# Kernel tuning notes

Hardware: AMD Instinct MI355X
Metric: run time of the kernel (lower is better)

The kernel has to match this reference:

```python
import jax, jax.numpy as jnp
import numpy as np

B, T, D = 2, 2048, 1024
K, F = 8, 4096
LAMBDA = 0.5


def setup_inputs() -> dict:
    key = jax.random.key(0)
    ks = jax.random.split(key, 8)
    s = 0.02
    return {
        "x": jax.random.normal(ks[0], (B, T, D), dtype=jnp.float32),
        "prev_logits": jax.random.normal(ks[1], (B, T, K), dtype=jnp.float32),
        "Wt": jax.random.normal(ks[2], (D, K), dtype=jnp.float32) * s,
        "Wgt": jax.random.normal(ks[3], (K, K), dtype=jnp.float32) * s,
        "We_logits": jnp.zeros((K,), dtype=jnp.float32),
        "W1": jax.random.normal(ks[4], (K, D, F), dtype=jnp.float32) * s,
        "b1": jnp.zeros((K, F), dtype=jnp.float32),
        "W2": jax.random.normal(ks[5], (K, F, D), dtype=jnp.float32) * s,
        "b2": jnp.zeros((K, D), dtype=jnp.float32),
    }


def reference(x, prev_logits, Wt, Wgt, We_logits, W1, b1, W2, b2):
    # gating: softmax over router logits, sigmoid-threshold multi-hot mask
    logits = jnp.einsum("btd,dk->btk", x, Wt) + jnp.einsum("btk,kj->btj", prev_logits, Wgt)
    st = jax.nn.softmax(logits, axis=-1)                       # (B,T,K)
    We = jax.nn.sigmoid(We_logits)                             # (K,)
    mask = (st > LAMBDA * We).astype(x.dtype)                  # (B,T,K)
    g = st * mask
    sel_counts = mask.sum(axis=(0, 1))                         # (K,)
    avg_density = mask.sum(axis=-1).mean()                     # scalar

    # dense multi-expert FFN: every expert on every token (dropout=0 / eval)
    h = jax.nn.gelu(jnp.einsum("btd,kdf->bktf", x, W1) + b1[:, None, :], approximate=False)
    outk = jnp.einsum("bktf,kfd->bktd", h, W2) + b2[:, None, :]  # (B,K,T,D)
    y = jnp.einsum("btk,bktd->btd", g, outk)
    y = y / (g.sum(axis=-1, keepdims=True) + 1e-6)
    return y, jax.lax.stop_gradient(logits), sel_counts, avg_density
```

## Files before the change

kernel.cpp:

```cpp
#include <hip/hip_runtime.h>
#include <cstdint>
#include <cstddef>

#define NB 2
#define NTT 2048
#define ND 1024
#define NK 8
#define NF 4096
#define NTOK (NB*NTT)
#define LAMBDA_C 0.5f

#define Y_SZ   (NTOK*ND)
#define LG_OFF Y_SZ
#define SC_OFF (LG_OFF + NTOK*NK)
#define AD_OFF (SC_OFF + NK)

#define WS_CNT    0
#define WS_SEG    8
#define WS_NTILES 17
#define WS_TILEK  32
#define WS_TILER  1056
#define WS_PTOK   4096
#define WS_PCOEF  36864
#define WS_COEF   69632
#define WS_X16    102400
#define WS_H      2199552

#define BM 128
#define BN 128
#define BK 64
#define SPLITK2 4

typedef float  f32x4 __attribute__((ext_vector_type(4)));
typedef _Float16 f16x8 __attribute__((ext_vector_type(8)));
typedef unsigned int u32x2 __attribute__((ext_vector_type(2)));
typedef unsigned int u32x4 __attribute__((ext_vector_type(4)));

__device__ __forceinline__ unsigned int pkrtz(float a, float b){
    auto h = __builtin_amdgcn_cvt_pkrtz(a, b);
    return __builtin_bit_cast(unsigned int, h);
}
__device__ __forceinline__ float gelu_exact(float v){
    return 0.5f * v * (1.0f + erff(v * 0.70710678118654752440f));
}

__global__ __launch_bounds__(256) void k_xcast(const float* __restrict__ x,
                                               unsigned short* __restrict__ x16)
{
    int i = (blockIdx.x*256 + threadIdx.x) * 16;
    const f32x4* src = (const f32x4*)(x + i);
    f32x4 v0 = src[0], v1 = src[1], v2 = src[2], v3 = src[3];
    u32x4 o0 = {pkrtz(v0[0],v0[1]), pkrtz(v0[2],v0[3]), pkrtz(v1[0],v1[1]), pkrtz(v1[2],v1[3])};
    u32x4 o1 = {pkrtz(v2[0],v2[1]), pkrtz(v2[2],v2[3]), pkrtz(v3[0],v3[1]), pkrtz(v3[2],v3[3])};
    *(u32x4*)(x16 + i)     = o0;
    *(u32x4*)(x16 + i + 8) = o1;
}

__global__ __launch_bounds__(256) void k_gating(
    const float* __restrict__ x, const float* __restrict__ pl,
    const float* __restrict__ Wt, const float* __restrict__ Wgt,
    const float* __restrict__ Wel, float* __restrict__ out,
    float* __restrict__ coef, int* __restrict__ cnt)
{
    int t = blockIdx.x;
    const float* xt = x + (size_t)t * ND;
    float acc[NK] = {0,0,0,0,0,0,0,0};
    for (int d = threadIdx.x; d < ND; d += 256){
        float xv = xt[d];
        const float4* w = (const float4*)(Wt + (size_t)d * NK);
        float4 w0 = w[0], w1 = w[1];
        acc[0] += xv*w0.x; acc[1] += xv*w0.y; acc[2] += xv*w0.z; acc[3] += xv*w0.w;
        acc[4] += xv*w1.x; acc[5] += xv*w1.y; acc[6] += xv*w1.z; acc[7] += xv*w1.w;
    }
    __shared__ float red[4][NK];
    #pragma unroll
    for (int k = 0; k < NK; k++){
        float v = acc[k];
        #pragma unroll
        for (int off = 32; off; off >>= 1) v += __shfl_down(v, off);
        if ((threadIdx.x & 63) == 0) red[threadIdx.x >> 6][k] = v;
    }
    __syncthreads();
    if (threadIdx.x == 0){
        const float* p = pl + (size_t)t * NK;
        float pv[NK];
        #pragma unroll
        for (int j = 0; j < NK; j++) pv[j] = p[j];
        float lg[NK]; float mx = -1e30f;
        #pragma unroll
        for (int k = 0; k < NK; k++){
            float v = red[0][k] + red[1][k] + red[2][k] + red[3][k];
            #pragma unroll
            for (int j = 0; j < NK; j++) v += pv[j] * Wgt[j*NK + k];
            lg[k] = v; mx = fmaxf(mx, v);
            out[LG_OFF + (size_t)t*NK + k] = v;
        }
        float e[NK]; float s = 0.f;
        #pragma unroll
        for (int k = 0; k < NK; k++){ e[k] = expf(lg[k] - mx); s += e[k]; }
        float g[NK]; float gsum = 0.f;
        #pragma unroll
        for (int k = 0; k < NK; k++){
            float st = e[k] / s;
            float we = 1.f / (1.f + expf(-Wel[k]));
            bool m = st > LAMBDA_C * we;
            g[k] = m ? st : 0.f;
            gsum += g[k];
        }
        float inv = 1.f / (gsum + 1e-6f);
        #pragma unroll
        for (int k = 0; k < NK; k++){
            coef[(size_t)t*NK + k] = g[k] * inv;
            if (g[k] > 0.f) atomicAdd(&cnt[k], 1);
        }
    }
}

__global__ __launch_bounds__(256) void k_scan(
    const float* __restrict__ coef, int* __restrict__ wsi,
    float* __restrict__ wsf, int pair_cap)
{
    int k = blockIdx.x;
    const int* cnt = wsi + WS_CNT;
    int base = 0;
    for (int j = 0; j < k; j++) base += cnt[j];
    int tid = threadIdx.x, lane = tid & 63, w = tid >> 6;
    __shared__ int wsum[4];
    __shared__ int sbase;
    if (tid == 0){
        sbase = base;
        wsi[WS_SEG + k] = base;
        if (k == NK-1) wsi[WS_SEG + NK] = base + cnt[k];
    }
    __syncthreads();
    int* ptok = wsi + WS_PTOK;
    float* pc = wsf + WS_PCOEF;
    for (int c0 = 0; c0 < NTOK; c0 += 256){
        int t = c0 + tid;
        float c = coef[(size_t)t*NK + k];
        bool m = c > 0.f;
        unsigned long long bal = __ballot(m);
        int pre = __popcll(bal & ((1ull << lane) - 1ull));
        if (lane == 0) wsum[w] = __popcll(bal);
        __syncthreads();
        int b = sbase;
        for (int j = 0; j < w; j++) b += wsum[j];
        if (m){
            int pos = b + pre;
            if (pos < pair_cap){ ptok[pos] = t; pc[pos] = c; }
        }
        __syncthreads();
        if (tid == 0) sbase += wsum[0] + wsum[1] + wsum[2] + wsum[3];
        __syncthreads();
    }
}

__global__ void k_tiles(int* __restrict__ wsi, float* __restrict__ out, int pair_cap)
{
    if (threadIdx.x == 0 && blockIdx.x == 0){
        const int* cnt = wsi + WS_CNT;
        const int* seg = wsi + WS_SEG;
        int total = 0;
        for (int k = 0; k < NK; k++){ total += cnt[k]; out[SC_OFF + k] = (float)cnt[k]; }
        out[AD_OFF] = (float)total / (float)NTOK;
        int nt = 0;
        for (int k = 0; k < NK; k++){
            int e = min(seg[k+1], pair_cap);
            for (int r = seg[k]; r < e; r += BM){
                wsi[WS_TILEK + nt] = k; wsi[WS_TILER + nt] = r; nt++;
            }
        }
        wsi[WS_NTILES] = nt;
    }
}

#define XCD_PART_LOOP(nwork)                                              \
    int q_ = (nwork) >> 3, rr_ = (nwork) & 7;                             \
    int xcd_ = blockIdx.x & 7;                                            \
    int slot_ = blockIdx.x >> 3;                                          \
    int nslot_ = gridDim.x >> 3;                                          \
    int cntw_ = q_ + (xcd_ < rr_ ? 1 : 0);                                \
    int start_ = xcd_ * q_ + (xcd_ < rr_ ? xcd_ : rr_);                   \
    for (int p_ = slot_; p_ < cntw_; p_ += nslot_)

#define LOAD_A16(ptr_)                                                    \
    { _Pragma("unroll")                                                   \
      for (int g_ = 0; g_ < 4; g_++) pa[g_] = *(const u32x4*)((ptr_) + g_*8); }

#define STAGE_A_F16()                                                     \
    { _Pragma("unroll")                                                   \
      for (int g_ = 0; g_ < 4; g_++){                                     \
          unsigned off_ = ((unsigned)((axkh*4 + g_)*16)) ^ aswz;          \
          *(u32x4*)(&lds[arowb + off_]) = pa[g_];                         \
      } }

#define STAGE_B_CVT(lb_)                                                  \
    {                                                                     \
        _Pragma("unroll")                                                 \
        for (int i_ = 0; i_ < 2; i_++){                                   \
            unsigned wA_[4], wB_[4];                                      \
            _Pragma("unroll")                                             \
            for (int r2_ = 0; r2_ < 4; r2_++){                            \
                wA_[r2_] = pkrtz(lb_[i_*4+r2_][0], lb_[i_*4+r2_][1]);     \
                wB_[r2_] = pkrtz(lb_[i_*4+r2_][2], lb_[i_*4+r2_][3]);     \
            }                                                             \
            unsigned kq8_ = (unsigned)((bk4 + i_*8) * 8);                 \
            _Pragma("unroll")                                             \
            for (int j_ = 0; j_ < 4; j_++){                               \
                unsigned s0_ = (j_ < 2) ? wA_[1] : wB_[1];                \
                unsigned s1_ = (j_ < 2) ? wA_[0] : wB_[0];                \
                unsigned s2_ = (j_ < 2) ? wA_[3] : wB_[3];                \
                unsigned s3_ = (j_ < 2) ? wA_[2] : wB_[2];                \
                unsigned sel_ = (j_ & 1) ? 0x07060302u : 0x05040100u;     \
                unsigned o0_ = __builtin_amdgcn_perm(s0_, s1_, sel_);     \
                unsigned o1_ = __builtin_amdgcn_perm(s2_, s3_, sel_);     \
                unsigned fswz_ = (unsigned)(((bf4*4 + j_) & 7) << 4);     \
                *(u32x2*)(&lds[bro + (unsigned)j_*128u + (kq8_ ^ fswz_)]) = (u32x2){o0_, o1_}; \
            }                                                             \
        }                                                                 \
    }

#define MFMA_STEP128()                                                    \
    {                                                                     \
        _Pragma("unroll")                                                 \
        for (int kk_ = 0; kk_ < 2; kk_++){                                \
            unsigned sb_ = ((unsigned)(kk_*64) + qk16) ^ swzL;            \
            f16x8 af_[4], bf_[4];                                         \
            _Pragma("unroll")                                             \
            for (int m_ = 0; m_ < 4; m_++) af_[m_] = *(const f16x8*)(&lds[abase + (unsigned)m_*2048u + sb_]); \
            _Pragma("unroll")                                             \
            for (int n_ = 0; n_ < 4; n_++) bf_[n_] = *(const f16x8*)(&lds[bbase + (unsigned)n_*2048u + sb_]); \
            _Pragma("unroll")                                             \
            for (int m_ = 0; m_ < 4; m_++)                                \
            _Pragma("unroll")                                             \
            for (int n_ = 0; n_ < 4; n_++)                                \
                acc[m_][n_] = __builtin_amdgcn_mfma_f32_16x16x32_f16(af_[m_], bf_[n_], acc[m_][n_], 0, 0, 0); \
        }                                                                 \
    }

#define LOAD_B(dst_, tt_, LDW_)                                           \
    { const float* bn_ = bp + (size_t)(tt_)*BK*LDW_;                      \
      _Pragma("unroll")                                                   \
      for (int i_ = 0; i_ < 2; i_++)                                      \
      _Pragma("unroll")                                                   \
      for (int r2_ = 0; r2_ < 4; r2_++)                                   \
          dst_[i_*4+r2_] = *(const f32x4*)(bn_ + (size_t)((bk4 + i_*8)*4 + r2_)*LDW_); }

__global__ __launch_bounds__(256, 2) void k_gemm1(
    const unsigned short* __restrict__ x16, const float* __restrict__ W1,
    const float* __restrict__ b1, const int* __restrict__ wsi,
    unsigned short* __restrict__ hbuf, int pair_cap)
{
    __shared__ char lds[32768];
    __shared__ int stok[BM];
    const int* seg  = wsi + WS_SEG;
    const int* tk   = wsi + WS_TILEK;
    const int* tr   = wsi + WS_TILER;
    const int* ptok = wsi + WS_PTOK;
    int ntm = wsi[WS_NTILES];
    int nwork = ntm * (NF / BN);
    int tid  = threadIdx.x;
    int lane = tid & 63;
    int w    = tid >> 6;
    int wr = w >> 1, wc = w & 1;
    int l15 = lane & 15, q = lane >> 4;
    unsigned swzL = (unsigned)((l15 & 7) << 4);
    unsigned qk16 = (unsigned)(q << 4);
    unsigned abase = (unsigned)(wr*64 + l15) * 128u;
    unsigned bbase = 16384u + (unsigned)(wc*64 + l15) * 128u;
    int axrow = tid >> 1, axkh = tid & 1;
    unsigned arowb = (unsigned)axrow * 128u;
    unsigned aswz  = (unsigned)((axrow & 7) << 4);
    int bk4 = tid & 7, bf4 = tid >> 3;
    unsigned bro = 16384u + (unsigned)(bf4*4) * 128u;

    XCD_PART_LOOP(nwork){
        int widx = start_ + p_;
        int mt = widx % ntm;
        int ft = widx / ntm;
        int kexp = tk[mt];
        int row0 = tr[mt];
        int nrows = min(BM, seg[kexp+1] - row0);
        int f0 = ft * BN;
        __syncthreads();
        if (tid < BM){
            int r = row0 + tid;
            stok[tid] = (tid < nrows && r < pair_cap) ? ptok[r] : ptok[row0];
        }
        __syncthreads();
        const unsigned short* xrow = x16 + (size_t)stok[axrow]*ND + axkh*32;
        const float* bp = W1 + (size_t)kexp*ND*NF + f0 + bf4*4;
        u32x4 pa[4]; f32x4 pb[8];
        LOAD_A16(xrow) LOAD_B(pb, 0, NF)
        f32x4 acc[4][4] = {};
        for (int t = 0; t < ND/BK; t++){
            if (t) __syncthreads();
            STAGE_A_F16() STAGE_B_CVT(pb)
            __syncthreads();
            if (t + 1 < ND/BK){
                const unsigned short* xn = xrow + (t+1)*BK;
                LOAD_A16(xn) LOAD_B(pb, t+1, NF)
            }
            MFMA_STEP128()
        }
        const float* b1k = b1 + (size_t)kexp*NF;
        #pragma unroll
        for (int n = 0; n < 4; n++){
            int f = f0 + wc*64 + n*16 + l15;
            float bv = b1k[f];
            #pragma unroll
            for (int m = 0; m < 4; m++){
                int rl = wr*64 + m*16 + q*4;
                #pragma unroll
                for (int i = 0; i < 4; i++){
                    int r = rl + i;
                    if (r < nrows && row0 + r < pair_cap){
                        float v = gelu_exact(acc[m][n][i] + bv);
                        hbuf[(size_t)(row0+r)*NF + f] = (unsigned short)(pkrtz(v, 0.f) & 0xffffu);
                    }
                }
            }
        }
    }
}

__global__ __launch_bounds__(256, 2) void k_gemm2(
    const unsigned short* __restrict__ hbuf, const float* __restrict__ W2,
    const float* __restrict__ b2, const int* __restrict__ wsi,
    const float* __restrict__ wsf, float* __restrict__ out, int pair_cap)
{
    __shared__ char lds[32768];
    __shared__ int stok[BM];
    __shared__ float scoef[BM];
    const int* seg  = wsi + WS_SEG;
    const int* tk   = wsi + WS_TILEK;
    const int* tr   = wsi + WS_TILER;
    const int* ptok = wsi + WS_PTOK;
    const float* pcoef = wsf + WS_PCOEF;
    int ntm = wsi[WS_NTILES];
    int nwork = ntm * (ND / BN) * SPLITK2;
    int tid  = threadIdx.x;
    int lane = tid & 63;
    int w    = tid >> 6;
    int wr = w >> 1, wc = w & 1;
    int l15 = lane & 15, q = lane >> 4;
    unsigned swzL = (unsigned)((l15 & 7) << 4);
    unsigned qk16 = (unsigned)(q << 4);
    unsigned abase = (unsigned)(wr*64 + l15) * 128u;
    unsigned bbase = 16384u + (unsigned)(wc*64 + l15) * 128u;
    int axrow = tid >> 1, axkh = tid & 1;
    unsigned arowb = (unsigned)axrow * 128u;
    unsigned aswz  = (unsigned)((axrow & 7) << 4);
    int bk4 = tid & 7, bf4 = tid >> 3;
    unsigned bro = 16384u + (unsigned)(bf4*4) * 128u;
    const int KT = (NF / SPLITK2) / BK;

    XCD_PART_LOOP(nwork){
        int widx = start_ + p_;
        int mt = widx % ntm;
        int rest = widx / ntm;
        int dt = rest & 7;
        int sp = rest >> 3;
        int kexp = tk[mt];
        int row0 = tr[mt];
        int nrows = min(BM, seg[kexp+1] - row0);
        int d0 = dt * BN;
        __syncthreads();
        if (tid < BM){
            int r = row0 + tid;
            bool v = (tid < nrows && r < pair_cap);
            stok[tid]  = v ? ptok[r] : 0;
            scoef[tid] = v ? pcoef[r] : 0.f;
        }
        __syncthreads();
        const unsigned short* hrow = hbuf + (size_t)min(row0 + axrow, pair_cap-1)*NF + sp*(NF/SPLITK2) + axkh*32;
        const float* bp = W2 + (size_t)kexp*NF*ND + (size_t)sp*(NF/SPLITK2)*ND + d0 + bf4*4;
        u32x4 pa[4]; f32x4 pb[8];
        LOAD_A16(hrow) LOAD_B(pb, 0, ND)
        f32x4 acc[4][4] = {};
        for (int t = 0; t < KT; t++){
            if (t) __syncthreads();
            STAGE_A_F16() STAGE_B_CVT(pb)
            __syncthreads();
            if (t + 1 < KT){
                const unsigned short* hn = hrow + (t+1)*BK;
                LOAD_A16(hn) LOAD_B(pb, t+1, ND)
            }
            MFMA_STEP128()
        }
        const float* b2k = b2 + (size_t)kexp*ND;
        #pragma unroll
        for (int n = 0; n < 4; n++){
            int d = d0 + wc*64 + n*16 + l15;
            float bv = (sp == 0) ? b2k[d] : 0.f;
            #pragma unroll
            for (int m = 0; m < 4; m++){
                int rl = wr*64 + m*16 + q*4;
                #pragma unroll
                for (int i = 0; i < 4; i++){
                    int r = rl + i;
                    if (r < nrows && row0 + r < pair_cap){
                        float c = scoef[r];
                        atomicAdd(&out[(size_t)stok[r]*ND + d], c * (acc[m][n][i] + bv));
                    }
                }
            }
        }
    }
}

extern "C" void kernel_launch(void* const* d_in, const int* in_sizes, int n_in,
                              void* d_out, int out_size, void* d_ws, size_t ws_size,
                              hipStream_t stream)
{
    const float* x   = (const float*)d_in[0];
    const float* pl  = (const float*)d_in[1];
    const float* Wt  = (const float*)d_in[2];
    const float* Wgt = (const float*)d_in[3];
    const float* Wel = (const float*)d_in[4];
    const float* W1  = (const float*)d_in[5];
    const float* b1  = (const float*)d_in[6];
    const float* W2  = (const float*)d_in[7];
    const float* b2  = (const float*)d_in[8];
    float* out = (float*)d_out;
    int* wsi   = (int*)d_ws;
    float* wsf = (float*)d_ws;
    unsigned short* x16  = (unsigned short*)((char*)d_ws + (size_t)WS_X16*4);
    unsigned short* hbuf = (unsigned short*)((char*)d_ws + (size_t)WS_H*4);

    long long avail = (long long)ws_size - (long long)WS_H*4;
    long long cap = avail / ((long long)NF*2);
    if (cap > (long long)NTOK*NK) cap = (long long)NTOK*NK;
    if (cap < 0) cap = 0;
    int pair_cap = (int)cap;

    hipMemsetAsync(d_out, 0, (size_t)out_size*sizeof(float), stream);
    hipMemsetAsync(d_ws, 0, 32, stream);
    k_xcast<<<1024, 256, 0, stream>>>(x, x16);
    k_gating<<<NTOK, 256, 0, stream>>>(x, pl, Wt, Wgt, Wel, out, wsf + WS_COEF, wsi + WS_CNT);
    if (pair_cap > 0){
        k_scan<<<NK, 256, 0, stream>>>(wsf + WS_COEF, wsi, wsf, pair_cap);
        k_tiles<<<1, 64, 0, stream>>>(wsi, out, pair_cap);
        k_gemm1<<<2048, 256, 0, stream>>>(x16, W1, b1, wsi, hbuf, pair_cap);
        k_gemm2<<<2048, 256, 0, stream>>>(hbuf, W2, b2, wsi, wsf, out, pair_cap);
    }
}
```

Measured before the change: 303.9 us.

## Double-buffer LDS with two-stage prefetch and narrower N tiles in expert GEMMs

Both expert GEMMs move from a single LDS buffer with two barriers per k-step to two LDS buffers, with global prefetch two k-steps ahead. Each step now uses one lgkmcnt wait plus a barrier. The N tile shrinks from 128 to 64 and launch bounds rise to 3 blocks per SM, trading per-block reuse for more tiles and higher occupancy. The aim is to hide global-load and conversion latency behind MFMA work and cut barrier stalls. The cost is double the reads of the gathered A operand and more atomic output work blocks in the second GEMM.

```diff
diff --git a/kernel.cpp b/kernel.cpp
--- a/kernel.cpp
+++ b/kernel.cpp
@@ -27,9 +27,15 @@
 #define WS_H      2199552
 
 #define BM 128
-#define BN 128
+#define BN 64
 #define BK 64
 #define SPLITK2 4
+#define KT 16
+
+#define AOFF0 0u
+#define AOFF1 16384u
+#define BOFF0 32768u
+#define BOFF1 40960u
 
 typedef float  f32x4 __attribute__((ext_vector_type(4)));
 typedef _Float16 f16x8 __attribute__((ext_vector_type(8)));
@@ -183,75 +189,76 @@
     int start_ = xcd_ * q_ + (xcd_ < rr_ ? xcd_ : rr_);                   \
     for (int p_ = slot_; p_ < cntw_; p_ += nslot_)
 
-#define LOAD_A16(ptr_)                                                    \
+
+#define LOAD_A(dst_, tt_)                                                 \
+    { const unsigned short* an_ = asrc + (tt_)*BK;                        \
+      _Pragma("unroll")                                                   \
+      for (int j_ = 0; j_ < 4; j_++) dst_[j_] = *(const u32x4*)(an_ + j_*8); }
+
+#define LOAD_B(dst_, tt_, LDW_)                                           \
+    { const float* bn_ = bsrc + (size_t)((tt_)*BK + bkq*4)*LDW_;          \
+      _Pragma("unroll")                                                   \
+      for (int r_ = 0; r_ < 4; r_++) dst_[r_] = *(const f32x4*)(bn_ + (size_t)r_*LDW_); }
+
+#define STAGE_A(src_, AO_)                                                \
     { _Pragma("unroll")                                                   \
-      for (int g_ = 0; g_ < 4; g_++) pa[g_] = *(const u32x4*)((ptr_) + g_*8); }
-
-#define STAGE_A_F16()                                                     \
+      for (int j_ = 0; j_ < 4; j_++){                                     \
+          unsigned off_ = (AO_) + (unsigned)arow*128u +                   \
+              ((((unsigned)(ahalf*4 + j_)) ^ (unsigned)(arow & 7)) << 4); \
+          *(u32x4*)(&lds[off_]) = src_[j_];                               \
+      } }
+
+#define STAGE_B(src_, BO_)                                                \
+    { unsigned wA_[4], wB_[4];                                            \
+      _Pragma("unroll")                                                   \
+      for (int r_ = 0; r_ < 4; r_++){                                     \
+          wA_[r_] = pkrtz(src_[r_][0], src_[r_][1]);                      \
+          wB_[r_] = pkrtz(src_[r_][2], src_[r_][3]);                      \
+      }                                                                   \
+      _Pragma("unroll")                                                   \
+      for (int j_ = 0; j_ < 4; j_++){                                     \
+          unsigned s0_ = (j_ < 2) ? wA_[1] : wB_[1];                      \
+          unsigned s1_ = (j_ < 2) ? wA_[0] : wB_[0];                      \
+          unsigned s2_ = (j_ < 2) ? wA_[3] : wB_[3];                      \
+          unsigned s3_ = (j_ < 2) ? wA_[2] : wB_[2];                      \
+          unsigned sel_ = (j_ & 1) ? 0x07060302u : 0x05040100u;           \
+          unsigned o0_ = __builtin_amdgcn_perm(s0_, s1_, sel_);           \
+          unsigned o1_ = __builtin_amdgcn_perm(s2_, s3_, sel_);           \
+          unsigned col_ = (unsigned)(bcc*4 + j_);                         \
+          unsigned off_ = (BO_) + col_*128u +                             \
+              (((unsigned)(bkq*8)) ^ ((col_ & 7u) << 4));                 \
+          *(u32x2*)(&lds[off_]) = (u32x2){o0_, o1_};                      \
+      } }
+
+#define MFMA_RD(AO_, BO_)                                                 \
     { _Pragma("unroll")                                                   \
-      for (int g_ = 0; g_ < 4; g_++){                                     \
-          unsigned off_ = ((unsigned)((axkh*4 + g_)*16)) ^ aswz;          \
-          *(u32x4*)(&lds[arowb + off_]) = pa[g_];                         \
+      for (int kk_ = 0; kk_ < 2; kk_++){                                  \
+          unsigned sb_ = ((unsigned)(kk_*64 + q*16)) ^ swzL;              \
+          f16x8 af_[4], bf_[2];                                           \
+          _Pragma("unroll")                                               \
+          for (int m_ = 0; m_ < 4; m_++)                                  \
+              af_[m_] = *(const f16x8*)(&lds[(AO_) + (unsigned)(wr*64 + m_*16 + l15)*128u + sb_]); \
+          _Pragma("unroll")                                               \
+          for (int n_ = 0; n_ < 2; n_++)                                  \
+              bf_[n_] = *(const f16x8*)(&lds[(BO_) + (unsigned)(wc*32 + n_*16 + l15)*128u + sb_]); \
+          _Pragma("unroll")                                               \
+          for (int m_ = 0; m_ < 4; m_++)                                  \
+          _Pragma("unroll")                                               \
+          for (int n_ = 0; n_ < 2; n_++)                                  \
+              acc[m_][n_] = __builtin_amdgcn_mfma_f32_16x16x32_f16(af_[m_], bf_[n_], acc[m_][n_], 0, 0, 0); \
       } }
 
-#define STAGE_B_CVT(lb_)                                                  \
-    {                                                                     \
-        _Pragma("unroll")                                                 \
-        for (int i_ = 0; i_ < 2; i_++){                                   \
-            unsigned wA_[4], wB_[4];                                      \
-            _Pragma("unroll")                                             \
-            for (int r2_ = 0; r2_ < 4; r2_++){                            \
-                wA_[r2_] = pkrtz(lb_[i_*4+r2_][0], lb_[i_*4+r2_][1]);     \
-                wB_[r2_] = pkrtz(lb_[i_*4+r2_][2], lb_[i_*4+r2_][3]);     \
-            }                                                             \
-            unsigned kq8_ = (unsigned)((bk4 + i_*8) * 8);                 \
-            _Pragma("unroll")                                             \
-            for (int j_ = 0; j_ < 4; j_++){                               \
-                unsigned s0_ = (j_ < 2) ? wA_[1] : wB_[1];                \
-                unsigned s1_ = (j_ < 2) ? wA_[0] : wB_[0];                \
-                unsigned s2_ = (j_ < 2) ? wA_[3] : wB_[3];                \
-                unsigned s3_ = (j_ < 2) ? wA_[2] : wB_[2];                \
-                unsigned sel_ = (j_ & 1) ? 0x07060302u : 0x05040100u;     \
-                unsigned o0_ = __builtin_amdgcn_perm(s0_, s1_, sel_);     \
-                unsigned o1_ = __builtin_amdgcn_perm(s2_, s3_, sel_);     \
-                unsigned fswz_ = (unsigned)(((bf4*4 + j_) & 7) << 4);     \
-                *(u32x2*)(&lds[bro + (unsigned)j_*128u + (kq8_ ^ fswz_)]) = (u32x2){o0_, o1_}; \
-            }                                                             \
-        }                                                                 \
-    }
-
-#define MFMA_STEP128()                                                    \
-    {                                                                     \
-        _Pragma("unroll")                                                 \
-        for (int kk_ = 0; kk_ < 2; kk_++){                                \
-            unsigned sb_ = ((unsigned)(kk_*64) + qk16) ^ swzL;            \
-            f16x8 af_[4], bf_[4];                                         \
-            _Pragma("unroll")                                             \
-            for (int m_ = 0; m_ < 4; m_++) af_[m_] = *(const f16x8*)(&lds[abase + (unsigned)m_*2048u + sb_]); \
-            _Pragma("unroll")                                             \
-            for (int n_ = 0; n_ < 4; n_++) bf_[n_] = *(const f16x8*)(&lds[bbase + (unsigned)n_*2048u + sb_]); \
-            _Pragma("unroll")                                             \
-            for (int m_ = 0; m_ < 4; m_++)                                \
-            _Pragma("unroll")                                             \
-            for (int n_ = 0; n_ < 4; n_++)                                \
-                acc[m_][n_] = __builtin_amdgcn_mfma_f32_16x16x32_f16(af_[m_], bf_[n_], acc[m_][n_], 0, 0, 0); \
-        }                                                                 \
-    }
-
-#define LOAD_B(dst_, tt_, LDW_)                                           \
-    { const float* bn_ = bp + (size_t)(tt_)*BK*LDW_;                      \
-      _Pragma("unroll")                                                   \
-      for (int i_ = 0; i_ < 2; i_++)                                      \
-      _Pragma("unroll")                                                   \
-      for (int r2_ = 0; r2_ < 4; r2_++)                                   \
-          dst_[i_*4+r2_] = *(const f32x4*)(bn_ + (size_t)((bk4 + i_*8)*4 + r2_)*LDW_); }
-
-__global__ __launch_bounds__(256, 2) void k_gemm1(
+#define STEP_SYNC()                                                       \
+    asm volatile("s_waitcnt lgkmcnt(0)" ::: "memory");                    \
+    __builtin_amdgcn_s_barrier();                                         \
+    __builtin_amdgcn_sched_barrier(0);
+
+__global__ __launch_bounds__(256, 3) void k_gemm1(
     const unsigned short* __restrict__ x16, const float* __restrict__ W1,
     const float* __restrict__ b1, const int* __restrict__ wsi,
     unsigned short* __restrict__ hbuf, int pair_cap)
 {
-    __shared__ char lds[32768];
+    __shared__ char lds[49152];
     __shared__ int stok[BM];
     const int* seg  = wsi + WS_SEG;
     const int* tk   = wsi + WS_TILEK;
@@ -265,14 +272,8 @@
     int wr = w >> 1, wc = w & 1;
     int l15 = lane & 15, q = lane >> 4;
     unsigned swzL = (unsigned)((l15 & 7) << 4);
-    unsigned qk16 = (unsigned)(q << 4);
-    unsigned abase = (unsigned)(wr*64 + l15) * 128u;
-    unsigned bbase = 16384u + (unsigned)(wc*64 + l15) * 128u;
-    int axrow = tid >> 1, axkh = tid & 1;
-    unsigned arowb = (unsigned)axrow * 128u;
-    unsigned aswz  = (unsigned)((axrow & 7) << 4);
-    int bk4 = tid & 7, bf4 = tid >> 3;
-    unsigned bro = 16384u + (unsigned)(bf4*4) * 128u;
+    int arow = tid >> 1, ahalf = tid & 1;
+    int bkq = tid >> 4, bcc = tid & 15;
 
     XCD_PART_LOOP(nwork){
         int widx = start_ + p_;
@@ -288,25 +289,26 @@
             stok[tid] = (tid < nrows && r < pair_cap) ? ptok[r] : ptok[row0];
         }
         __syncthreads();
-        const unsigned short* xrow = x16 + (size_t)stok[axrow]*ND + axkh*32;
-        const float* bp = W1 + (size_t)kexp*ND*NF + f0 + bf4*4;
-        u32x4 pa[4]; f32x4 pb[8];
-        LOAD_A16(xrow) LOAD_B(pb, 0, NF)
-        f32x4 acc[4][4] = {};
-        for (int t = 0; t < ND/BK; t++){
-            if (t) __syncthreads();
-            STAGE_A_F16() STAGE_B_CVT(pb)
-            __syncthreads();
-            if (t + 1 < ND/BK){
-                const unsigned short* xn = xrow + (t+1)*BK;
-                LOAD_A16(xn) LOAD_B(pb, t+1, NF)
-            }
-            MFMA_STEP128()
+        const unsigned short* asrc = x16 + (size_t)stok[arow]*ND + ahalf*32;
+        const float* bsrc = W1 + (size_t)kexp*ND*NF + f0 + bcc*4;
+        u32x4 ga0[4], ga1[4]; f32x4 gb0[4], gb1[4];
+        LOAD_A(ga0, 0) LOAD_B(gb0, 0, NF)
+        LOAD_A(ga1, 1) LOAD_B(gb1, 1, NF)
+        f32x4 acc[4][2] = {};
+        for (int t = 0; t < KT; t += 2){
+            STAGE_A(ga0, AOFF0) STAGE_B(gb0, BOFF0)
+            if (t + 2 < KT){ LOAD_A(ga0, t+2) LOAD_B(gb0, t+2, NF) }
+            STEP_SYNC()
+            MFMA_RD(AOFF0, BOFF0)
+            STAGE_A(ga1, AOFF1) STAGE_B(gb1, BOFF1)
+            if (t + 3 < KT){ LOAD_A(ga1, t+3) LOAD_B(gb1, t+3, NF) }
+            STEP_SYNC()
+            MFMA_RD(AOFF1, BOFF1)
         }
         const float* b1k = b1 + (size_t)kexp*NF;
         #pragma unroll
-        for (int n = 0; n < 4; n++){
-            int f = f0 + wc*64 + n*16 + l15;
+        for (int n = 0; n < 2; n++){
+            int f = f0 + wc*32 + n*16 + l15;
             float bv = b1k[f];
             #pragma unroll
             for (int m = 0; m < 4; m++){
@@ -324,12 +326,12 @@
     }
 }
 
-__global__ __launch_bounds__(256, 2) void k_gemm2(
+__global__ __launch_bounds__(256, 3) void k_gemm2(
     const unsigned short* __restrict__ hbuf, const float* __restrict__ W2,
     const float* __restrict__ b2, const int* __restrict__ wsi,
     const float* __restrict__ wsf, float* __restrict__ out, int pair_cap)
 {
-    __shared__ char lds[32768];
+    __shared__ char lds[49152];
     __shared__ int stok[BM];
     __shared__ float scoef[BM];
     const int* seg  = wsi + WS_SEG;
@@ -345,22 +347,15 @@
     int wr = w >> 1, wc = w & 1;
     int l15 = lane & 15, q = lane >> 4;
     unsigned swzL = (unsigned)((l15 & 7) << 4);
-    unsigned qk16 = (unsigned)(q << 4);
-    unsigned abase = (unsigned)(wr*64 + l15) * 128u;
-    unsigned bbase = 16384u + (unsigned)(wc*64 + l15) * 128u;
-    int axrow = tid >> 1, axkh = tid & 1;
-    unsigned arowb = (unsigned)axrow * 128u;
-    unsigned aswz  = (unsigned)((axrow & 7) << 4);
-    int bk4 = tid & 7, bf4 = tid >> 3;
-    unsigned bro = 16384u + (unsigned)(bf4*4) * 128u;
-    const int KT = (NF / SPLITK2) / BK;
+    int arow = tid >> 1, ahalf = tid & 1;
+    int bkq = tid >> 4, bcc = tid & 15;
 
     XCD_PART_LOOP(nwork){
         int widx = start_ + p_;
         int mt = widx % ntm;
         int rest = widx / ntm;
-        int dt = rest & 7;
-        int sp = rest >> 3;
+        int dt = rest & 15;
+        int sp = rest >> 4;
         int kexp = tk[mt];
         int row0 = tr[mt];
         int nrows = min(BM, seg[kexp+1] - row0);
@@ -373,25 +368,27 @@
             scoef[tid] = v ? pcoef[r] : 0.f;
         }
         __syncthreads();
-        const unsigned short* hrow = hbuf + (size_t)min(row0 + axrow, pair_cap-1)*NF + sp*(NF/SPLITK2) + axkh*32;
-        const float* bp = W2 + (size_t)kexp*NF*ND + (size_t)sp*(NF/SPLITK2)*ND + d0 + bf4*4;
-        u32x4 pa[4]; f32x4 pb[8];
-        LOAD_A16(hrow) LOAD_B(pb, 0, ND)
-        f32x4 acc[4][4] = {};
-        for (int t = 0; t < KT; t++){
-            if (t) __syncthreads();
-            STAGE_A_F16() STAGE_B_CVT(pb)
-            __syncthreads();
-            if (t + 1 < KT){
-                const unsigned short* hn = hrow + (t+1)*BK;
-                LOAD_A16(hn) LOAD_B(pb, t+1, ND)
-            }
-            MFMA_STEP128()
+        int hr = row0 + arow; if (hr >= pair_cap) hr = pair_cap - 1;
+        const unsigned short* asrc = hbuf + (size_t)hr*NF + sp*(NF/SPLITK2) + ahalf*32;
+        const float* bsrc = W2 + (size_t)kexp*NF*ND + (size_t)sp*(NF/SPLITK2)*ND + d0 + bcc*4;
+        u32x4 ga0[4], ga1[4]; f32x4 gb0[4], gb1[4];
+        LOAD_A(ga0, 0) LOAD_B(gb0, 0, ND)
+        LOAD_A(ga1, 1) LOAD_B(gb1, 1, ND)
+        f32x4 acc[4][2] = {};
+        for (int t = 0; t < KT; t += 2){
+            STAGE_A(ga0, AOFF0) STAGE_B(gb0, BOFF0)
+            if (t + 2 < KT){ LOAD_A(ga0, t+2) LOAD_B(gb0, t+2, ND) }
+            STEP_SYNC()
+            MFMA_RD(AOFF0, BOFF0)
+            STAGE_A(ga1, AOFF1) STAGE_B(gb1, BOFF1)
+            if (t + 3 < KT){ LOAD_A(ga1, t+3) LOAD_B(gb1, t+3, ND) }
+            STEP_SYNC()
+            MFMA_RD(AOFF1, BOFF1)
         }
         const float* b2k = b2 + (size_t)kexp*ND;
         #pragma unroll
-        for (int n = 0; n < 4; n++){
-            int d = d0 + wc*64 + n*16 + l15;
+        for (int n = 0; n < 2; n++){
+            int d = d0 + wc*32 + n*16 + l15;
             float bv = (sp == 0) ? b2k[d] : 0.f;
             #pragma unroll
             for (int m = 0; m < 4; m++){
```

New measurement: 244.7 us. -19.5%, faster.
